# Performance work log

Hardware: AMD Instinct MI355X
Metric: run time of the kernel (lower is better)

The kernel has to match this reference:

```python
import jax, jax.numpy as jnp
import numpy as np

B, S, D, H = 4, 1024, 1024, 16
DK = D // H


def setup_inputs() -> dict:
    key = jax.random.key(0)
    ks = jax.random.split(key, 8)
    scale = 1.0 / np.sqrt(D)
    inp = {
        "x": jax.random.normal(ks[0], (B, S, D), jnp.float32),
        "encoder_output": jax.random.normal(ks[1], (B, S, D), jnp.float32),
        "src_mask": jnp.ones((1, 1, 1, S), jnp.int32),
        "tgt_mask": jnp.tril(jnp.ones((S, S), jnp.int32))[None, None, :, :],
        "wq_self": jax.random.normal(ks[2], (D, D), jnp.float32) * scale,
        "wk_self": jax.random.normal(ks[3], (D, D), jnp.float32) * scale,
        "wv_self": jax.random.normal(ks[4], (D, D), jnp.float32) * scale,
        "wq_cross": jax.random.normal(ks[5], (D, D), jnp.float32) * scale,
        "wk_cross": jax.random.normal(ks[6], (D, D), jnp.float32) * scale,
        "wv_cross": jax.random.normal(ks[7], (D, D), jnp.float32) * scale,
    }
    return inp


def _mha(q_in, k_in, v_in, wq, wk, wv, mask):
    # nn.Linear (no bias): y = x @ W.T
    def split_heads(t):
        b, s, _ = t.shape
        return t.reshape(b, s, H, DK).transpose(0, 2, 1, 3)  # [B,H,S,DK]

    q = split_heads(q_in @ wq.T)
    k = split_heads(k_in @ wk.T)
    v = split_heads(v_in @ wv.T)
    scores = jnp.einsum("bhqd,bhkd->bhqk", q, k) / jnp.sqrt(jnp.float32(DK))
    scores = jnp.where(mask == 0, jnp.float32(-1e9), scores)
    attn = jax.nn.softmax(scores, axis=-1)
    out = jnp.einsum("bhqk,bhkd->bhqd", attn, v)  # [B,H,S,DK]
    return out.transpose(0, 2, 1, 3).reshape(q_in.shape[0], -1, H * DK)


def reference(x, encoder_output, src_mask, tgt_mask,
              wq_self, wk_self, wv_self, wq_cross, wk_cross, wv_cross):
    x = _mha(x, x, x, wq_self, wk_self, wv_self, tgt_mask)
    x = _mha(x, encoder_output, encoder_output, wq_cross, wk_cross, wv_cross, src_mask)
    return x
```

## Files before the change

### kernel.cpp

```cpp
#include <hip/hip_runtime.h>
#include <stdint.h>


typedef unsigned short u16;
typedef short b16x8 __attribute__((ext_vector_type(8)));
typedef short b16x4 __attribute__((ext_vector_type(4)));
typedef float f32x4 __attribute__((ext_vector_type(4)));

__device__ __forceinline__ u16 f2bf(float f) {
  union { float f; uint32_t u; } v; v.f = f;
  uint32_t r = v.u + 0x7fffu + ((v.u >> 16) & 1u);
  return (u16)(r >> 16);
}

__device__ __forceinline__ f32x4 mfma16(b16x8 a, b16x8 b, f32x4 c) {
  return __builtin_amdgcn_mfma_f32_16x16x32_bf16(a, b, c, 0, 0, 0);
}

__device__ __forceinline__ void gld16(const void* g, void* l) {
  __builtin_amdgcn_global_load_lds(
      (const __attribute__((address_space(1))) void*)g,
      (__attribute__((address_space(3))) void*)l, 16, 0, 0);
}

__device__ __forceinline__ float ex2(float x) {
  float r; asm("v_exp_f32 %0, %1" : "=v"(r) : "v"(x)); return r;
}

__device__ __forceinline__ uint32_t cvtpk(float a, float b) {
  uint32_t r;
  asm("v_cvt_pk_bf16_f32 %0, %1, %2" : "=v"(r) : "v"(a), "v"(b));
  return r;
}

__global__ __launch_bounds__(256) void k_cvt_all(
    const float* __restrict__ x, const float* __restrict__ enc,
    const float* __restrict__ w0, const float* __restrict__ w1,
    const float* __restrict__ w2, const float* __restrict__ w3,
    const float* __restrict__ w4, const float* __restrict__ w5,
    u16* __restrict__ xb, u16* __restrict__ encb,
    u16* __restrict__ wsc, u16* __restrict__ wcc) {
  const int id = blockIdx.x;
  const float* in;
  u16* out;
  float sc = 1.0f;
  int off;
  if (id < 2048) {
    in = x; out = xb; off = id;
  } else if (id < 4096) {
    in = enc; out = encb; off = id - 2048;
  } else {
    const int wi = (id - 4096) >> 9;
    off = (id - 4096) & 511;
    switch (wi) {
      case 0: in = w0; break; case 1: in = w1; break; case 2: in = w2; break;
      case 3: in = w3; break; case 4: in = w4; break; default: in = w5; break;
    }
    out = (wi < 3 ? wsc : wcc) + (wi % 3) * 1048576;
    if (wi % 3 == 0) sc = 0.18033688f;
  }
  const int i = (off * 256 + threadIdx.x) * 8;
  float4 a = *(const float4*)(in + i);
  float4 b = *(const float4*)(in + i + 4);
  b16x8 v;
  v[0] = (short)f2bf(a.x * sc); v[1] = (short)f2bf(a.y * sc);
  v[2] = (short)f2bf(a.z * sc); v[3] = (short)f2bf(a.w * sc);
  v[4] = (short)f2bf(b.x * sc); v[5] = (short)f2bf(b.y * sc);
  v[6] = (short)f2bf(b.z * sc); v[7] = (short)f2bf(b.w * sc);
  *(b16x8*)(out + i) = v;
}

__global__ __launch_bounds__(256) void k_gemm_bt(
    const u16* __restrict__ A0, const u16* __restrict__ B0,
    u16* __restrict__ C0, int N0, int nbx0,
    const u16* __restrict__ A1, const u16* __restrict__ B1,
    u16* __restrict__ C1, int N1) {
  __shared__ u16 Ab[128 * 32];
  __shared__ u16 Bb[128 * 32];
  const int tid = threadIdx.x;
  const int lane = tid & 63, w = tid >> 6;
  const int wr = w >> 1, wc = w & 1;
  const int q = lane & 15, hi = lane >> 4;
  const int nwg = gridDim.x * gridDim.y;
  const int id = blockIdx.y * gridDim.x + blockIdx.x;
  const int swz = (id & 7) * (nwg >> 3) + (id >> 3);
  const int bx = swz % gridDim.x, by = swz / gridDim.x;
  const u16* A; const u16* B; u16* C; int N, nb;
  if (bx < nbx0) { A = A0; B = B0; C = C0; N = N0; nb = bx; }
  else           { A = A1; B = B1; C = C1; N = N1; nb = bx - nbx0; }
  const int mbase = by * 128, nbase = nb * 128;
  f32x4 acc[4][4] = {};
  for (int kb = 0; kb < 1024; kb += 32) {
    __syncthreads();
#pragma unroll
    for (int r = 0; r < 2; ++r) {
      int c = tid + 256 * r;
      int row = c >> 2, ch = c & 3;
      gld16(&A[(size_t)(mbase + row) * 1024 + kb + ch * 8], &Ab[c * 8]);
      gld16(&B[(size_t)(nbase + row) * 1024 + kb + ch * 8], &Bb[c * 8]);
    }
    __syncthreads();
    b16x8 af[4], bf[4];
#pragma unroll
    for (int mi = 0; mi < 4; ++mi)
      af[mi] = *(const b16x8*)&Ab[(wr * 64 + mi * 16 + q) * 32 + hi * 8];
#pragma unroll
    for (int ni = 0; ni < 4; ++ni)
      bf[ni] = *(const b16x8*)&Bb[(wc * 64 + ni * 16 + q) * 32 + hi * 8];
#pragma unroll
    for (int mi = 0; mi < 4; ++mi)
#pragma unroll
      for (int ni = 0; ni < 4; ++ni)
        acc[mi][ni] = mfma16(bf[ni], af[mi], acc[mi][ni]);
  }
#pragma unroll
  for (int mi = 0; mi < 4; ++mi) {
    const int m = mbase + wr * 64 + mi * 16 + q;
#pragma unroll
    for (int ni = 0; ni < 4; ++ni) {
      const int nc = nbase + wc * 64 + ni * 16 + hi * 4;
      uint2 o;
      o.x = cvtpk(acc[mi][ni][0], acc[mi][ni][1]);
      o.y = cvtpk(acc[mi][ni][2], acc[mi][ni][3]);
      *(uint2*)&C[(size_t)m * N + nc] = o;
    }
  }
}

__global__ __launch_bounds__(256) void k_vt(const u16* __restrict__ in, int sIn,
                                            int coff, u16* __restrict__ out) {
  __shared__ u16 T[64 * 72];
  const int tid = threadIdx.x;
  const int bh = blockIdx.y, kb = blockIdx.x * 64;
  const int b = bh >> 4, h = bh & 15;
  const int kvp = tid >> 3, ch = tid & 7;
  const u16* p = in + (size_t)(b * 1024 + kb + 2 * kvp) * sIn + coff + h * 64 + ch * 8;
  b16x8 r0 = *(const b16x8*)p;
  b16x8 r1 = *(const b16x8*)(p + sIn);
#pragma unroll
  for (int j = 0; j < 8; ++j) {
    int i = (j + ch) & 7;
    uint32_t pk = (uint32_t)(u16)r0[i] | ((uint32_t)(u16)r1[i] << 16);
    *(uint32_t*)&T[(ch * 8 + i) * 72 + 2 * kvp] = pk;
  }
  __syncthreads();
  const int d = tid >> 2, seg = tid & 3;
  b16x8 v0 = *(const b16x8*)&T[d * 72 + seg * 16];
  b16x8 v1 = *(const b16x8*)&T[d * 72 + seg * 16 + 8];
  u16* o = out + (size_t)(bh * 64 + d) * 1024 + kb + seg * 16;
  *(b16x8*)o = v0;
  *(b16x8*)(o + 8) = v1;
}

template <int CAUSAL, typename OT>
__global__ __launch_bounds__(256, 3) void attn4(
    const u16* __restrict__ Qp, int sQ,
    const u16* __restrict__ Kp, int sK, int koff,
    const u16* __restrict__ Vt,
    OT* __restrict__ Op, int sO) {
  __shared__ u16 Ksh[2][64 * 64];
  __shared__ u16 Vsh[2][64 * 64];
  __shared__ u16 Plds[4][32 * 72];
  const int tid = threadIdx.x;
  const int lane = tid & 63, w = tid >> 6;
  const int lq = lane & 15, hi = lane >> 4;

  const int id = blockIdx.y * gridDim.x + blockIdx.x;
  const int xcd = id & 7, l = id >> 3;
  const int bh = xcd * 8 + (l >> 3);
  const int qb = (l < 32) ? (l & 7) : 7 - (l & 7);

  const size_t rowb = (size_t)(bh >> 4) * 1024;
  const int h = bh & 15;
  const int qw0 = qb * 128 + w * 32;
  const int nt = CAUSAL ? 2 * qb + 2 : 16;

  const u16* Kbase = Kp + rowb * (size_t)sK + koff + h * 64;
  const u16* Vbase = Vt + (size_t)bh * 65536;
  const u16* Qb = Qp + (rowb + qw0 + lq) * (size_t)sQ + h * 64 + hi * 8;
  u16* Pw = &Plds[w][0];

  b16x8 qf[2][2];
  qf[0][0] = *(const b16x8*)Qb;
  qf[0][1] = *(const b16x8*)(Qb + 32);
  qf[1][0] = *(const b16x8*)(Qb + (size_t)16 * sQ);
  qf[1][1] = *(const b16x8*)(Qb + (size_t)16 * sQ + 32);

  b16x8 ones;
#pragma unroll
  for (int i = 0; i < 8; ++i) ones[i] = (short)0x3F80;

  const int key = lq & 7;

  f32x4 acc[2][4] = {};
  f32x4 accl[2] = {};
  float m0 = -1e30f, m1 = -1e30f;

  auto stage = [&](int bf, int kt2) {
    const int kb2 = kt2 * 64;
#pragma unroll
    for (int r = 0; r < 2; ++r) {
      int c = tid + 256 * r;
      int row = c >> 3, ch = c & 7;
      int sw = row & 7;
      gld16(&Kbase[(size_t)(kb2 + row) * sK + ((ch ^ sw) << 3)],
            &Ksh[bf][c * 8]);
      gld16(&Vbase[(size_t)row * 1024 + kb2 + ((ch ^ sw) << 3)],
            &Vsh[bf][c * 8]);
    }
  };

  stage(0, 0);
  for (int kt = 0; kt < nt; ++kt) {
    __syncthreads();
    if (kt + 1 < nt) stage((kt + 1) & 1, kt + 1);
    const int kb = kt * 64;
    if (CAUSAL && kb > qw0 + 31) continue;
    const u16* Kl = Ksh[kt & 1];
    const u16* Vl = Vsh[kt & 1];

    f32x4 st[2][4];
#pragma unroll
    for (int t = 0; t < 4; ++t) {
      const int row = 16 * t + lq;
      b16x8 k0 = *(const b16x8*)&Kl[row * 64 + ((hi ^ key) << 3)];
      b16x8 k1 = *(const b16x8*)&Kl[row * 64 + (((4 + hi) ^ key) << 3)];
      f32x4 z0 = {}, z1 = {};
      z0 = mfma16(k0, qf[0][0], z0);
      st[0][t] = mfma16(k1, qf[0][1], z0);
      z1 = mfma16(k0, qf[1][0], z1);
      st[1][t] = mfma16(k1, qf[1][1], z1);
    }

    const bool dm = CAUSAL && (kb + 63 > qw0);
    float pm[2];
#pragma unroll
    for (int g = 0; g < 2; ++g) {
      if (dm) {
        const int qg = qw0 + g * 16 + lq;
#pragma unroll
        for (int t = 0; t < 4; ++t)
#pragma unroll
          for (int i = 0; i < 4; ++i)
            if (kb + 16 * t + 4 * hi + i > qg) st[g][t][i] = -INFINITY;
      }
      float m = -INFINITY;
#pragma unroll
      for (int t = 0; t < 4; ++t)
#pragma unroll
        for (int i = 0; i < 4; ++i) m = fmaxf(m, st[g][t][i]);
      m = fmaxf(m, __shfl_xor(m, 16));
      m = fmaxf(m, __shfl_xor(m, 32));
      pm[g] = m;
    }

    if (!__all((pm[0] <= m0 + 10.f) && (pm[1] <= m1 + 10.f))) {
      float n0 = fmaxf(m0, pm[0]), n1 = fmaxf(m1, pm[1]);
      float f0 = ex2(m0 - n0), f1 = ex2(m1 - n1);
#pragma unroll
      for (int t = 0; t < 4; ++t)
#pragma unroll
        for (int i = 0; i < 4; ++i) {
          acc[0][t][i] *= f0;
          acc[1][t][i] *= f1;
        }
#pragma unroll
      for (int i = 0; i < 4; ++i) { accl[0][i] *= f0; accl[1][i] *= f1; }
      m0 = n0; m1 = n1;
    }

#pragma unroll
    for (int g = 0; g < 2; ++g) {
      const float mm = g ? m1 : m0;
#pragma unroll
      for (int t = 0; t < 4; ++t) {
        uint2 pw;
        pw.x = cvtpk(ex2(st[g][t][0] - mm), ex2(st[g][t][1] - mm));
        pw.y = cvtpk(ex2(st[g][t][2] - mm), ex2(st[g][t][3] - mm));
        *(uint2*)&Pw[(g * 16 + lq) * 72 + 16 * t + 4 * hi] = pw;
      }
    }

    b16x8 av0[4], av1[4];
#pragma unroll
    for (int t = 0; t < 4; ++t) {
      const int rv = 16 * t + lq;
      av0[t] = *(const b16x8*)&Vl[rv * 64 + ((hi ^ key) << 3)];
      av1[t] = *(const b16x8*)&Vl[rv * 64 + (((4 + hi) ^ key) << 3)];
    }

#pragma unroll
    for (int g = 0; g < 2; ++g) {
      b16x8 bp0 = *(const b16x8*)&Pw[(g * 16 + lq) * 72 + hi * 8];
      b16x8 bp1 = *(const b16x8*)&Pw[(g * 16 + lq) * 72 + 32 + hi * 8];
      accl[g] = mfma16(ones, bp0, accl[g]);
      accl[g] = mfma16(ones, bp1, accl[g]);
#pragma unroll
      for (int t = 0; t < 4; ++t) {
        acc[g][t] = mfma16(av0[t], bp0, acc[g][t]);
        acc[g][t] = mfma16(av1[t], bp1, acc[g][t]);
      }
    }
  }

#pragma unroll
  for (int g = 0; g < 2; ++g) {
    const float inv = 1.0f / accl[g][0];
    const size_t ob = (rowb + qw0 + g * 16 + lq) * (size_t)sO + h * 64;
#pragma unroll
    for (int t = 0; t < 4; ++t) {
      const int d = 16 * t + 4 * hi;
      if constexpr (sizeof(OT) == 2) {
        b16x4 o;
        o[0] = (short)f2bf(acc[g][t][0] * inv);
        o[1] = (short)f2bf(acc[g][t][1] * inv);
        o[2] = (short)f2bf(acc[g][t][2] * inv);
        o[3] = (short)f2bf(acc[g][t][3] * inv);
        *(b16x4*)&((u16*)Op)[ob + d] = o;
      } else {
        float4 o = make_float4(acc[g][t][0] * inv, acc[g][t][1] * inv,
                               acc[g][t][2] * inv, acc[g][t][3] * inv);
        *(float4*)&((float*)Op)[ob + d] = o;
      }
    }
  }
}

extern "C" void kernel_launch(void* const* d_in, const int* in_sizes, int n_in,
                              void* d_out, int out_size, void* d_ws, size_t ws_size,
                              hipStream_t stream) {
  (void)in_sizes; (void)n_in; (void)out_size; (void)ws_size;
  const float* x   = (const float*)d_in[0];
  const float* enc = (const float*)d_in[1];
  const float* wqs = (const float*)d_in[4];
  const float* wks = (const float*)d_in[5];
  const float* wvs = (const float*)d_in[6];
  const float* wqc = (const float*)d_in[7];
  const float* wkc = (const float*)d_in[8];
  const float* wvc = (const float*)d_in[9];

  u16* ws   = (u16*)d_ws;
  u16* xb   = ws;
  u16* encb = ws + 4194304;
  u16* wsc  = ws + 8388608;
  u16* wcc  = ws + 11534336;
  u16* qkv1 = ws + 14680064;
  u16* x1b  = ws + 27262976;
  u16* q2   = ws + 31457280;
  u16* kv2  = ws + 35651584;

  k_cvt_all<<<7168, 256, 0, stream>>>(x, enc, wqs, wks, wvs, wqc, wkc, wvc,
                                      xb, encb, wsc, wcc);

  k_gemm_bt<<<dim3(24, 32), 256, 0, stream>>>(xb, wsc, qkv1, 3072, 24,
                                              xb, wsc, qkv1, 3072);
  k_vt<<<dim3(16, 64), 256, 0, stream>>>(qkv1, 3072, 2048, xb);
  attn4<1, u16><<<dim3(8, 64), 256, 0, stream>>>(
      qkv1, 3072, qkv1, 3072, 1024, xb, x1b, 1024);

  k_gemm_bt<<<dim3(24, 32), 256, 0, stream>>>(x1b, wcc, q2, 1024, 8,
                                              encb, wcc + 1048576, kv2, 2048);
  k_vt<<<dim3(16, 64), 256, 0, stream>>>(kv2, 2048, 1024, encb);
  attn4<0, float><<<dim3(8, 64), 256, 0, stream>>>(
      q2, 1024, kv2, 2048, 0, encb, (float*)d_out, 1024);
}
```

Before: 280.2 us.

## Fuse V transpose into GEMM epilogue and split cross-attention projection GEMMs

The GEMM epilogue now writes the V-projection columns directly in transposed [bh][d][kv] layout, which removes the separate k_vt transpose kernels and their extra global read/write pass. The MFMA operand order is swapped so each lane holds four consecutive rows, and the non-V outputs are stored as scalar bf16 writes. The cross-attention Q and KV projections now run as two separate launches instead of one merged grid, which adds a launch and shrinks each grid. The scalar strided stores in the normal epilogue may be less efficient than the previous packed 8-byte stores.

```diff
diff --git a/kernel.cpp b/kernel.cpp
--- a/kernel.cpp
+++ b/kernel.cpp
@@ -71,10 +71,8 @@
 }
 
 __global__ __launch_bounds__(256) void k_gemm_bt(
-    const u16* __restrict__ A0, const u16* __restrict__ B0,
-    u16* __restrict__ C0, int N0, int nbx0,
-    const u16* __restrict__ A1, const u16* __restrict__ B1,
-    u16* __restrict__ C1, int N1) {
+    const u16* __restrict__ A, const u16* __restrict__ B,
+    u16* __restrict__ C, int N, u16* __restrict__ vt, int vcol0) {
   __shared__ u16 Ab[128 * 32];
   __shared__ u16 Bb[128 * 32];
   const int tid = threadIdx.x;
@@ -85,10 +83,7 @@
   const int id = blockIdx.y * gridDim.x + blockIdx.x;
   const int swz = (id & 7) * (nwg >> 3) + (id >> 3);
   const int bx = swz % gridDim.x, by = swz / gridDim.x;
-  const u16* A; const u16* B; u16* C; int N, nb;
-  if (bx < nbx0) { A = A0; B = B0; C = C0; N = N0; nb = bx; }
-  else           { A = A1; B = B1; C = C1; N = N1; nb = bx - nbx0; }
-  const int mbase = by * 128, nbase = nb * 128;
+  const int mbase = by * 128, nbase = bx * 128;
   f32x4 acc[4][4] = {};
   for (int kb = 0; kb < 1024; kb += 32) {
     __syncthreads();
@@ -111,45 +106,37 @@
     for (int mi = 0; mi < 4; ++mi)
 #pragma unroll
       for (int ni = 0; ni < 4; ++ni)
-        acc[mi][ni] = mfma16(bf[ni], af[mi], acc[mi][ni]);
-  }
-#pragma unroll
-  for (int mi = 0; mi < 4; ++mi) {
-    const int m = mbase + wr * 64 + mi * 16 + q;
-#pragma unroll
-    for (int ni = 0; ni < 4; ++ni) {
-      const int nc = nbase + wc * 64 + ni * 16 + hi * 4;
-      uint2 o;
-      o.x = cvtpk(acc[mi][ni][0], acc[mi][ni][1]);
-      o.y = cvtpk(acc[mi][ni][2], acc[mi][ni][3]);
-      *(uint2*)&C[(size_t)m * N + nc] = o;
-    }
-  }
-}
-
-__global__ __launch_bounds__(256) void k_vt(const u16* __restrict__ in, int sIn,
-                                            int coff, u16* __restrict__ out) {
-  __shared__ u16 T[64 * 72];
-  const int tid = threadIdx.x;
-  const int bh = blockIdx.y, kb = blockIdx.x * 64;
-  const int b = bh >> 4, h = bh & 15;
-  const int kvp = tid >> 3, ch = tid & 7;
-  const u16* p = in + (size_t)(b * 1024 + kb + 2 * kvp) * sIn + coff + h * 64 + ch * 8;
-  b16x8 r0 = *(const b16x8*)p;
-  b16x8 r1 = *(const b16x8*)(p + sIn);
-#pragma unroll
-  for (int j = 0; j < 8; ++j) {
-    int i = (j + ch) & 7;
-    uint32_t pk = (uint32_t)(u16)r0[i] | ((uint32_t)(u16)r1[i] << 16);
-    *(uint32_t*)&T[(ch * 8 + i) * 72 + 2 * kvp] = pk;
-  }
-  __syncthreads();
-  const int d = tid >> 2, seg = tid & 3;
-  b16x8 v0 = *(const b16x8*)&T[d * 72 + seg * 16];
-  b16x8 v1 = *(const b16x8*)&T[d * 72 + seg * 16 + 8];
-  u16* o = out + (size_t)(bh * 64 + d) * 1024 + kb + seg * 16;
-  *(b16x8*)o = v0;
-  *(b16x8*)(o + 8) = v1;
+        acc[mi][ni] = mfma16(af[mi], bf[ni], acc[mi][ni]);
+  }
+  if (nbase >= vcol0) {
+    const int hc = nbase - vcol0;
+#pragma unroll
+    for (int mi = 0; mi < 4; ++mi) {
+      const int m0 = mbase + wr * 64 + mi * 16 + hi * 4;
+      const int bh16 = (m0 >> 10) * 16;
+      const int kv = m0 & 1023;
+#pragma unroll
+      for (int ni = 0; ni < 4; ++ni) {
+        const int n0 = hc + wc * 64 + ni * 16 + q;
+        const int bh = bh16 + (n0 >> 6), d = n0 & 63;
+        uint2 o;
+        o.x = cvtpk(acc[mi][ni][0], acc[mi][ni][1]);
+        o.y = cvtpk(acc[mi][ni][2], acc[mi][ni][3]);
+        *(uint2*)&vt[(size_t)bh * 65536 + d * 1024 + kv] = o;
+      }
+    }
+  } else {
+#pragma unroll
+    for (int mi = 0; mi < 4; ++mi)
+#pragma unroll
+      for (int ni = 0; ni < 4; ++ni) {
+        int m0 = mbase + wr * 64 + mi * 16 + hi * 4;
+        int n0 = nbase + wc * 64 + ni * 16 + q;
+#pragma unroll
+        for (int i = 0; i < 4; ++i)
+          C[(size_t)(m0 + i) * N + n0] = f2bf(acc[mi][ni][i]);
+      }
+  }
 }
 
 template <int CAUSAL, typename OT>
@@ -352,15 +339,13 @@
   k_cvt_all<<<7168, 256, 0, stream>>>(x, enc, wqs, wks, wvs, wqc, wkc, wvc,
                                       xb, encb, wsc, wcc);
 
-  k_gemm_bt<<<dim3(24, 32), 256, 0, stream>>>(xb, wsc, qkv1, 3072, 24,
-                                              xb, wsc, qkv1, 3072);
-  k_vt<<<dim3(16, 64), 256, 0, stream>>>(qkv1, 3072, 2048, xb);
+  k_gemm_bt<<<dim3(24, 32), 256, 0, stream>>>(xb, wsc, qkv1, 3072, q2, 2048);
   attn4<1, u16><<<dim3(8, 64), 256, 0, stream>>>(
-      qkv1, 3072, qkv1, 3072, 1024, xb, x1b, 1024);
-
-  k_gemm_bt<<<dim3(24, 32), 256, 0, stream>>>(x1b, wcc, q2, 1024, 8,
-                                              encb, wcc + 1048576, kv2, 2048);
-  k_vt<<<dim3(16, 64), 256, 0, stream>>>(kv2, 2048, 1024, encb);
+      qkv1, 3072, qkv1, 3072, 1024, q2, x1b, 1024);
+
+  k_gemm_bt<<<dim3(8, 32), 256, 0, stream>>>(x1b, wcc, q2, 1024, q2, 1 << 28);
+  k_gemm_bt<<<dim3(16, 32), 256, 0, stream>>>(encb, wcc + 1048576, kv2, 2048,
+                                              xb, 1024);
   attn4<0, float><<<dim3(8, 64), 256, 0, stream>>>(
-      q2, 1024, kv2, 2048, 0, encb, (float*)d_out, 1024);
-}
+      q2, 1024, kv2, 2048, 0, xb, (float*)d_out, 1024);
+}
```

New measurement: 273.3 us. 2.5% less time.

## Hoist cross-attention K/V projection into first GEMM launch and merge V transposes

Applied to the files above, without the earlier changes.

Folds the encoder K/V projection into the first self-attention QKV GEMM launch, growing its grid from 24 to 40 column tiles so one launch does more independent work. The two V-transpose kernels become a single launch selected by blockIdx.y. The later GEMM then only computes the cross-attention Q projection. The GEMM epilogue also swaps the MFMA operand order and writes scalar bf16 elements down columns instead of packed row stores, which may weaken store coalescing.

```diff
diff --git a/kernel.cpp b/kernel.cpp
--- a/kernel.cpp
+++ b/kernel.cpp
@@ -111,27 +111,30 @@
     for (int mi = 0; mi < 4; ++mi)
 #pragma unroll
       for (int ni = 0; ni < 4; ++ni)
-        acc[mi][ni] = mfma16(bf[ni], af[mi], acc[mi][ni]);
-  }
-#pragma unroll
-  for (int mi = 0; mi < 4; ++mi) {
-    const int m = mbase + wr * 64 + mi * 16 + q;
+        acc[mi][ni] = mfma16(af[mi], bf[ni], acc[mi][ni]);
+  }
+#pragma unroll
+  for (int mi = 0; mi < 4; ++mi)
 #pragma unroll
     for (int ni = 0; ni < 4; ++ni) {
-      const int nc = nbase + wc * 64 + ni * 16 + hi * 4;
-      uint2 o;
-      o.x = cvtpk(acc[mi][ni][0], acc[mi][ni][1]);
-      o.y = cvtpk(acc[mi][ni][2], acc[mi][ni][3]);
-      *(uint2*)&C[(size_t)m * N + nc] = o;
-    }
-  }
-}
-
-__global__ __launch_bounds__(256) void k_vt(const u16* __restrict__ in, int sIn,
-                                            int coff, u16* __restrict__ out) {
+      int m0 = mbase + wr * 64 + mi * 16 + hi * 4;
+      int n0 = nbase + wc * 64 + ni * 16 + q;
+#pragma unroll
+      for (int i = 0; i < 4; ++i)
+        C[(size_t)(m0 + i) * N + n0] = f2bf(acc[mi][ni][i]);
+    }
+}
+
+__global__ __launch_bounds__(256) void k_vt2x(
+    const u16* __restrict__ in0, int s0, int c0, u16* __restrict__ out0,
+    const u16* __restrict__ in1, int s1, int c1, u16* __restrict__ out1) {
   __shared__ u16 T[64 * 72];
   const int tid = threadIdx.x;
-  const int bh = blockIdx.y, kb = blockIdx.x * 64;
+  const int sel = blockIdx.y >> 6;
+  const u16* in = sel ? in1 : in0;
+  u16* out = sel ? out1 : out0;
+  const int sIn = sel ? s1 : s0, coff = sel ? c1 : c0;
+  const int bh = blockIdx.y & 63, kb = blockIdx.x * 64;
   const int b = bh >> 4, h = bh & 15;
   const int kvp = tid >> 3, ch = tid & 7;
   const u16* p = in + (size_t)(b * 1024 + kb + 2 * kvp) * sIn + coff + h * 64 + ch * 8;
@@ -352,15 +355,18 @@
   k_cvt_all<<<7168, 256, 0, stream>>>(x, enc, wqs, wks, wvs, wqc, wkc, wvc,
                                       xb, encb, wsc, wcc);
 
-  k_gemm_bt<<<dim3(24, 32), 256, 0, stream>>>(xb, wsc, qkv1, 3072, 24,
-                                              xb, wsc, qkv1, 3072);
-  k_vt<<<dim3(16, 64), 256, 0, stream>>>(qkv1, 3072, 2048, xb);
+  k_gemm_bt<<<dim3(40, 32), 256, 0, stream>>>(xb, wsc, qkv1, 3072, 24,
+                                              encb, wcc + 1048576, kv2, 2048);
+
+  k_vt2x<<<dim3(16, 128), 256, 0, stream>>>(qkv1, 3072, 2048, xb,
+                                            kv2, 2048, 1024, encb);
+
   attn4<1, u16><<<dim3(8, 64), 256, 0, stream>>>(
       qkv1, 3072, qkv1, 3072, 1024, xb, x1b, 1024);
 
-  k_gemm_bt<<<dim3(24, 32), 256, 0, stream>>>(x1b, wcc, q2, 1024, 8,
-                                              encb, wcc + 1048576, kv2, 2048);
-  k_vt<<<dim3(16, 64), 256, 0, stream>>>(kv2, 2048, 1024, encb);
+  k_gemm_bt<<<dim3(8, 32), 256, 0, stream>>>(x1b, wcc, q2, 1024, 8,
+                                             x1b, wcc, q2, 1024);
+
   attn4<0, float><<<dim3(8, 64), 256, 0, stream>>>(
       q2, 1024, kv2, 2048, 0, encb, (float*)d_out, 1024);
 }
```

Result: faster. 258.3 us (-7.8%).
